# Performance work log

Measured on AMD Instinct MI355X. Metric: run time of the kernel, lower is better.

The kernel has to match this reference:

```python
import jax, jax.numpy as jnp
import numpy as np

LEAKY_ALPHA = 0.2  # LeakyReLU negative slope from init arg `alpha`


def setup_inputs() -> dict:
    key = jax.random.key(0)
    k1, k2, k3, k4 = jax.random.split(key, 4)
    B, N, Fin, Fout = 8, 2048, 256, 256
    h = jax.random.normal(k1, (B, N, Fin), dtype=jnp.float32)
    adj = jax.random.randint(k2, (N, N), 0, 2, dtype=jnp.int32)
    W = jax.random.normal(k3, (Fin, Fout), dtype=jnp.float32) * (1.414 * (6.0 / (Fin + Fout)) ** 0.5)
    a = jax.random.normal(k4, (2 * Fout, 1), dtype=jnp.float32) * (1.414 * (6.0 / (2 * Fout + 1)) ** 0.5)
    return {"h": h, "adj": adj, "W": W, "a": a}


def reference(h, adj, W, a):
    # h: (B, N, Fin), adj: (N, N) int {0,1}, W: (Fin, Fout), a: (2*Fout, 1)
    Fout = W.shape[1]
    Wh = jnp.einsum('bnf,fo->bno', h, W)            # (B, N, Fout)
    a1 = a[:Fout, 0]                                  # attends to target node i
    a2 = a[Fout:, 0]                                  # attends to source node j
    # a^T [Wh_i || Wh_j] == (Wh_i . a1) + (Wh_j . a2); LeakyReLU applied after, as in original
    s_i = Wh @ a1                                     # (B, N)
    s_j = Wh @ a2                                     # (B, N)
    e = jax.nn.leaky_relu(s_i[:, :, None] + s_j[:, None, :], negative_slope=LEAKY_ALPHA)  # (B, N, N)
    N = Wh.shape[1]
    mask = (adj > 0) | jnp.eye(N, dtype=bool)         # adjacency + self-loops
    e = jnp.where(mask[None, :, :], e, -jnp.inf)
    attention = jax.nn.softmax(e, axis=-1)            # dropout is identity in eval
    attention = jnp.nan_to_num(attention, nan=0.0)
    h_prime = jnp.einsum('bij,bjo->bio', attention, Wh)  # (B, N, Fout)
    return jax.nn.elu(h_prime)                        # concat=True -> ELU
```

## Files before the change

kernel.cpp:

```cpp
#include <hip/hip_runtime.h>

typedef unsigned short u16;
typedef unsigned int   u32;
typedef unsigned long long u64;

typedef __bf16 bf16x8 __attribute__((ext_vector_type(8)));
typedef float  f32x4  __attribute__((ext_vector_type(4)));
typedef float  f32x16 __attribute__((ext_vector_type(16)));

#define MFMA_BF16(a,b,c)   __builtin_amdgcn_mfma_f32_16x16x32_bf16((a),(b),(c),0,0,0)
#define MFMA32_BF16(a,b,c) __builtin_amdgcn_mfma_f32_32x32x16_bf16((a),(b),(c),0,0,0)

__device__ __forceinline__ float bf2f(u16 u) {
    return __uint_as_float(((u32)u) << 16);
}
__device__ __forceinline__ u16 f2bf(float x) {
    u32 u = __float_as_uint(x);
    u += 0x7fffu + ((u >> 16) & 1u);
    return (u16)(u >> 16);
}
__device__ __forceinline__ float ldany(const void* p, size_t i, int f32) {
    return f32 ? ((const float*)p)[i] : bf2f(((const u16*)p)[i]);
}
__device__ __forceinline__ int detect_f32(const u32* hw) {
    u32 w = hw[threadIdx.x & 63];
    int e = (w >> 23) & 0xFF;
    u64 m = __ballot(e >= 64 && e <= 190);
    return __popcll(m) >= 32 ? 1 : 0;
}
__device__ __forceinline__ void lbar() {
    asm volatile("s_waitcnt lgkmcnt(0)" ::: "memory");
    __builtin_amdgcn_s_barrier();
}

__global__ __launch_bounds__(256) void kprep0(const void* __restrict__ w, const void* __restrict__ a,
                                              u16* __restrict__ wt, float* __restrict__ wa1,
                                              float* __restrict__ wa2, int* __restrict__ cnt,
                                              const u32* __restrict__ hw) {
    __shared__ float s1[4], s2[4];
    int bid = blockIdx.x, t = threadIdx.x;
    int wid = t >> 6, lane = t & 63;
    if (bid == 0 && t < 8) cnt[t] = 0;
    int f32 = detect_f32(hw);
    int k = bid, o = t;
    float wv = ldany(w, (size_t)k * 256 + o, f32);
    wt[o * 256 + k] = f2bf(wv);
    float p1 = wv * ldany(a, o, f32);
    float p2 = wv * ldany(a, 256 + o, f32);
    for (int d = 32; d; d >>= 1) { p1 += __shfl_down(p1, d); p2 += __shfl_down(p2, d); }
    if (lane == 0) { s1[wid] = p1; s2[wid] = p2; }
    __syncthreads();
    if (o == 0) { wa1[k] = s1[0] + s1[1] + s1[2] + s1[3]; wa2[k] = s2[0] + s2[1] + s2[2] + s2[3]; }
}

struct __align__(16) K2LDS {
    u16 At[64 * 68];
    union { u16 Bt[256 * 68]; u16 Ct[256 * 68]; };
    float wa1s[256], wa2s[256];
    float s1[64], s2[64];
};
__global__ __launch_bounds__(1024, 4) void k2m(const void* __restrict__ h, const u16* __restrict__ wt,
                                               const float* __restrict__ wa1, const float* __restrict__ wa2,
                                               u16* __restrict__ whbt,
                                               float* __restrict__ sig, float* __restrict__ sjg,
                                               const int* __restrict__ adj, u64* __restrict__ mb64) {
    __shared__ K2LDS L;
    int bid = blockIdx.x;
    int t = threadIdx.x;
    int wid = t >> 6, lane = t & 63, ln = lane & 15, qd = lane >> 4;

    if (bid >= 256) {
        int w2 = (bid - 256) * 16 + wid;
        int4 v[8];
        #pragma unroll
        for (int s = 0; s < 8; s++) {
            int task = w2 * 8 + s;
            int row = task >> 3, jb = (task & 7) * 256;
            v[s] = *(const int4*)(adj + (size_t)row * 2048 + jb + lane * 4);
        }
        #pragma unroll
        for (int s = 0; s < 8; s++) {
            int task = w2 * 8 + s;
            int row = task >> 3, jb = (task & 7) * 256;
            int j0 = jb + lane * 4;
            u32 nib = (u32)(v[s].x > 0 || j0     == row)
                    | ((u32)(v[s].y > 0 || j0 + 1 == row) << 1)
                    | ((u32)(v[s].z > 0 || j0 + 2 == row) << 2)
                    | ((u32)(v[s].w > 0 || j0 + 3 == row) << 3);
            u32 sh = 4 * (lane & 7);
            u32 lo = (lane & 8) ? 0u : (nib << sh);
            u32 hi = (lane & 8) ? (nib << sh) : 0u;
            #pragma unroll
            for (int d = 1; d <= 8; d <<= 1) {
                lo |= __shfl_xor(lo, d);
                hi |= __shfl_xor(hi, d);
            }
            if ((lane & 15) == 0)
                mb64[(size_t)row * 32 + (jb >> 6) + (lane >> 4)] =
                    (u64)lo | ((u64)hi << 32);
        }
        return;
    }

    int f32 = detect_f32((const u32*)h);
    int m0 = bid * 64;
    int b  = m0 >> 11;
    int n0 = m0 & 2047;

    if (t < 256) { L.wa1s[t] = wa1[t]; L.wa2s[t] = wa2[t]; }
    if (t < 64) { L.s1[t] = 0.f; L.s2[t] = 0.f; }
    __syncthreads();

    float a1 = 0.f, a2 = 0.f;
    f32x4 acc[4];
    for (int mi = 0; mi < 4; mi++) acc[mi] = (f32x4){0.f, 0.f, 0.f, 0.f};

    for (int c = 0; c < 4; c++) {
        int k0c = c * 64;
        if (t < 512) {
            int r = t >> 3, s = t & 7;
            float xv[8]; u16 uv[8];
            if (f32) {
                const float* src = (const float*)h + (size_t)(m0 + r) * 256 + k0c + s * 8;
                f32x4 x0 = *(const f32x4*)src;
                f32x4 x1 = *(const f32x4*)(src + 4);
                #pragma unroll
                for (int q = 0; q < 4; q++) { xv[q] = x0[q]; xv[4 + q] = x1[q]; }
                #pragma unroll
                for (int q = 0; q < 8; q++) uv[q] = f2bf(xv[q]);
            } else {
                const u16* src = (const u16*)h + (size_t)(m0 + r) * 256 + k0c + s * 8;
                *(uint4*)uv = *(const uint4*)src;
                #pragma unroll
                for (int q = 0; q < 8; q++) xv[q] = bf2f(uv[q]);
            }
            *(uint4*)&L.At[r * 68 + s * 8] = *(uint4*)uv;
            float pa = 0.f, pb = 0.f;
            #pragma unroll
            for (int q = 0; q < 8; q++) {
                pa += xv[q] * L.wa1s[k0c + s * 8 + q];
                pb += xv[q] * L.wa2s[k0c + s * 8 + q];
            }
            a1 += pa; a2 += pb;
        } else {
            int tt = t - 512;
            #pragma unroll
            for (int p = 0; p < 4; p++) {
                int f = (tt >> 3) + p * 64, s = tt & 7;
                *(uint4*)&L.Bt[f * 68 + s * 8] =
                    *(const uint4*)(wt + (size_t)f * 256 + k0c + s * 8);
            }
        }
        __syncthreads();
        for (int ks = 0; ks < 2; ks++) {
            bf16x8 af[4], bfr;
            for (int mi = 0; mi < 4; mi++)
                af[mi] = *(const bf16x8*)&L.At[(mi * 16 + ln) * 68 + ks * 32 + qd * 8];
            bfr = *(const bf16x8*)&L.Bt[(wid * 16 + ln) * 68 + ks * 32 + qd * 8];
            for (int mi = 0; mi < 4; mi++)
                acc[mi] = MFMA_BF16(af[mi], bfr, acc[mi]);
        }
        __syncthreads();
    }

    if (t < 512) {
        atomicAdd(&L.s1[t >> 3], a1);
        atomicAdd(&L.s2[t >> 3], a2);
    }
    for (int mi = 0; mi < 4; mi++) {
        int f = wid * 16 + ln;
        int n = mi * 16 + qd * 4;
        u16 v[4];
        for (int r = 0; r < 4; r++) v[r] = f2bf(acc[mi][r]);
        *(uint2*)&L.Ct[f * 68 + n] = *(uint2*)v;
    }
    __syncthreads();
    if (t < 64) { sig[m0 + t] = L.s1[t]; sjg[m0 + t] = L.s2[t]; }
    {
        int fr = t >> 2, q0 = (t & 3) * 2;
        size_t base = (size_t)b * 524288 + (size_t)fr * 2048 + n0;
        #pragma unroll
        for (int k = 0; k < 2; k++) {
            int s = q0 + k;
            uint4 v = *(uint4*)&L.Ct[fr * 68 + s * 8];
            *(uint4*)(whbt + base + s * 8) = v;
        }
    }
}

struct __align__(16) K4LDS {
    u32   vpack[2048];
    u16   sjb[2048];
    u64   mw[64 * 33];
    float u1[64], u2[64], nsi[64], inv[64];
    float lred[1024];
    u16   Pt[2][8192];
    int   claim[2];
    u32   pad1blk[4096];
};
__global__ __launch_bounds__(1024, 4) void k4(const float* __restrict__ sig,
                                              const float* __restrict__ sjg,
                                              const u64* __restrict__ mb64, const u16* __restrict__ whbt,
                                              void* __restrict__ out, const void* __restrict__ hdet,
                                              int* __restrict__ cnt) {
    __shared__ K4LDS L;
    int f32 = detect_f32((const u32*)hdet);
    int t = threadIdx.x;
    if (t == 0) {
        int xcd = __builtin_amdgcn_s_getreg(63508) & 7;
        int bsel = 0, tile = 0;
        #pragma unroll
        for (int k = 0; k < 8; k++) {
            int bb = (xcd + k) & 7;
            int tt = atomicAdd(&cnt[bb], 1);
            if (tt < 32) { bsel = bb; tile = tt; break; }
        }
        L.claim[0] = bsel; L.claim[1] = tile;
    }
    __syncthreads();
    int b  = L.claim[0];
    int i0 = L.claim[1] * 64;
    int wid = t >> 6, lane = t & 63;
    int l31 = lane & 31, h5 = lane >> 5;
    int fg = wid & 7, ig = wid >> 3;
    const u16* wb = whbt + (size_t)b * 524288 + (size_t)fg * 32 * 2048;
    float lacc = 0.f;

    bf16x8 br[2][8];
    #define LOAD_B(cc, bb) do {                                             \
        int j0_ = (cc) * 128;                                               \
        _Pragma("unroll")                                                   \
        for (int ks = 0; ks < 8; ks++)                                      \
            br[bb][ks] = *(const bf16x8*)(wb +                              \
                (size_t)l31 * 2048 + j0_ + ks * 16 + h5 * 8);               \
    } while (0)

    #define PGEN(cc, bb) do {                                               \
        int r_ = t & 63, o_ = t >> 6;                                       \
        int jb_ = (cc) * 128 + o_ * 8;                                      \
        uint4 pkA_ = *(const uint4*)&L.vpack[jb_];                          \
        uint4 pkB_ = *(const uint4*)&L.vpack[jb_ + 4];                      \
        uint4 sj4_ = *(const uint4*)&L.sjb[jb_];                            \
        u32 mb_ = (u32)(L.mw[r_ * 33 + 2 * (cc) + (o_ >> 3)]                \
                        >> ((o_ & 7) * 8)) & 0xffu;                         \
        float u1_ = L.u1[r_], u2_ = L.u2[r_], nsi_ = L.nsi[r_];             \
        u32 pr_[4];                                                         \
        _Pragma("unroll")                                                   \
        for (int pk = 0; pk < 4; pk++) {                                    \
            u32 vw0_ = (pk == 0) ? pkA_.x : (pk == 1) ? pkA_.z              \
                     : (pk == 2) ? pkB_.x : pkB_.z;                         \
            u32 vw1_ = (pk == 0) ? pkA_.y : (pk == 1) ? pkA_.w              \
                     : (pk == 2) ? pkB_.y : pkB_.w;                         \
            u32 sw_ = (pk == 0) ? sj4_.x : (pk == 1) ? sj4_.y               \
                     : (pk == 2) ? sj4_.z : sj4_.w;                         \
            float sj0_ = __uint_as_float(sw_ << 16);                        \
            float sj1_ = __uint_as_float(sw_ & 0xffff0000u);                \
            float p0_, p1_;                                                 \
            {                                                               \
                bool pos = sj0_ > nsi_;                                     \
                float vv = __uint_as_float(pos ? (vw0_ << 16)               \
                                               : ((vw0_ >> 16) << 16));     \
                p0_ = (pos ? u1_ : u2_) * vv;                               \
                p0_ = ((mb_ >> (2 * pk)) & 1u) ? p0_ : 0.f;                 \
            }                                                               \
            {                                                               \
                bool pos = sj1_ > nsi_;                                     \
                float vv = __uint_as_float(pos ? (vw1_ << 16)               \
                                               : ((vw1_ >> 16) << 16));     \
                p1_ = (pos ? u1_ : u2_) * vv;                               \
                p1_ = ((mb_ >> (2 * pk + 1)) & 1u) ? p1_ : 0.f;             \
            }                                                               \
            lacc += p0_ + p1_;                                              \
            pr_[pk] = __builtin_amdgcn_perm(__float_as_uint(p1_),           \
                                            __float_as_uint(p0_),           \
                                            0x07060302u);                   \
        }                                                                   \
        *(uint4*)&L.Pt[bb][t * 8] = *(uint4*)pr_;                           \
    } while (0)

    LOAD_B(0, 0);
    float sjv0 = sjg[b * 2048 + t];
    float sjv1 = sjg[b * 2048 + 1024 + t];
    {
        float mx = fmaxf(sjv0, sjv1);
        for (int d = 32; d; d >>= 1) mx = fmaxf(mx, __shfl_xor(mx, d));
        if (lane == 0) L.lred[wid] = mx;
    }
    for (int p = 0; p < 2; p++) {
        int idx = t + p * 1024;
        int r = idx >> 5, c = idx & 31;
        L.mw[r * 33 + c] = mb64[(size_t)(i0 + r) * 32 + c];
    }
    __syncthreads();
    float Mb;
    {
        float m0_ = fmaxf(fmaxf(fmaxf(L.lred[0], L.lred[1]), fmaxf(L.lred[2], L.lred[3])),
                          fmaxf(fmaxf(L.lred[4], L.lred[5]), fmaxf(L.lred[6], L.lred[7])));
        float m1_ = fmaxf(fmaxf(fmaxf(L.lred[8], L.lred[9]), fmaxf(L.lred[10], L.lred[11])),
                          fmaxf(fmaxf(L.lred[12], L.lred[13]), fmaxf(L.lred[14], L.lred[15])));
        Mb = fmaxf(m0_, m1_);
    }
    {
        float vj0 = __expf(sjv0 - Mb), v2j0 = __expf(0.2f * (sjv0 - Mb));
        L.vpack[t] = (u32)f2bf(vj0) | ((u32)f2bf(v2j0) << 16);
        L.sjb[t] = f2bf(sjv0);
        float vj1 = __expf(sjv1 - Mb), v2j1 = __expf(0.2f * (sjv1 - Mb));
        L.vpack[t + 1024] = (u32)f2bf(vj1) | ((u32)f2bf(v2j1) << 16);
        L.sjb[t + 1024] = f2bf(sjv1);
    }
    if (t < 64) {
        float siv = sig[b * 2048 + i0 + t];
        float x = siv + Mb;
        float K = fmaxf(x, 0.2f * x);
        L.u1[t] = __expf(x - K);
        L.u2[t] = __expf(0.2f * x - K);
        L.nsi[t] = -siv;
    }
    __syncthreads();
    PGEN(0, 0);

    f32x16 acc;
    #pragma unroll
    for (int q = 0; q < 16; q++) acc[q] = 0.f;

    #define STEP(c, cur, nxt) do {                                          \
        lbar();                                                             \
        if ((c) < 15) { LOAD_B((c) + 1, nxt); PGEN((c) + 1, nxt); }         \
        __builtin_amdgcn_s_setprio(1);                                      \
        _Pragma("unroll")                                                   \
        for (int ks = 0; ks < 8; ks++) {                                    \
            bf16x8 af = *(const bf16x8*)&L.Pt[cur][((ks * 2 + h5) * 64 +    \
                                                    ig * 32 + l31) * 8];    \
            acc = MFMA32_BF16(af, br[cur][ks], acc);                        \
        }                                                                   \
        __builtin_amdgcn_s_setprio(0);                                      \
    } while (0)

    for (int cc = 0; cc < 8; cc++) {
        STEP(2 * cc,     0, 1);
        STEP(2 * cc + 1, 1, 0);
    }

    __syncthreads();
    L.lred[t] = lacc;
    __syncthreads();
    if (t < 64) {
        float s = 0.f;
        #pragma unroll
        for (int q = 0; q < 16; q++) s += L.lred[q * 64 + t];
        L.inv[t] = 1.0f / s;
    }
    __syncthreads();

    {
        int fcol = fg * 32 + l31;
        #pragma unroll
        for (int reg = 0; reg < 16; reg++) {
            int il = ig * 32 + (reg & 3) + 8 * (reg >> 2) + 4 * h5;
            float hp = acc[reg] * L.inv[il];
            float y = hp > 0.f ? hp : (__expf(hp) - 1.f);
            size_t idx = (size_t)(b * 2048 + i0 + il) * 256 + fcol;
            if (f32) ((float*)out)[idx] = y;
            else     ((u16*)out)[idx]   = f2bf(y);
        }
    }
    #undef LOAD_B
    #undef PGEN
    #undef STEP
}

extern "C" void kernel_launch(void* const* d_in, const int* in_sizes, int n_in,
                              void* d_out, int out_size, void* d_ws, size_t ws_size,
                              hipStream_t stream) {
    const void* h   = d_in[0];
    const int*  adj = (const int*)d_in[1];
    const void* W   = d_in[2];
    const void* a   = d_in[3];

    char* ws = (char*)d_ws;
    u16*   WT    = (u16*)  (ws + 0);
    float* si    = (float*)(ws + 131072);
    float* sj    = (float*)(ws + 196608);
    u64*   mb64  = (u64*)  (ws + 557056);
    u16*   whbt  = (u16*)  (ws + 1081344);
    float* Wa1   = (float*)(ws + 9469952);
    float* Wa2   = (float*)(ws + 9470976);
    int*   cnt   = (int*)  (ws + 9472000);

    kprep0<<<dim3(256), dim3(256),  0, stream>>>(W, a, WT, Wa1, Wa2, cnt, (const u32*)h);
    k2m   <<<dim3(384), dim3(1024), 0, stream>>>(h, WT, Wa1, Wa2, whbt, si, sj, adj, mb64);
    k4    <<<dim3(256), dim3(1024), 0, stream>>>(si, sj, mb64, whbt, d_out, h, cnt);
}
```

Before: 161.2 us.

## Move adjacency bitmask packing into prep kernel and simplify k4 barrier

Adjacency-to-bitmask packing moves out of the second kernel into the first prep kernel. It now runs as 2048 small 256-thread blocks doing two tasks per wave, next to the W transpose blocks, so the projection GEMM kernel launches only its 256 tiles. The k4 launch-bounds occupancy hint is dropped, and the custom lgkmcnt-wait-plus-barrier is replaced by __syncthreads. The aim is to stop the mask work from competing with the GEMM tiles and to spread it over more blocks. The risks are a heavier prep kernel and possibly looser register or occupancy settings for k4.

```diff
diff --git a/kernel.cpp b/kernel.cpp
--- a/kernel.cpp
+++ b/kernel.cpp
@@ -28,60 +28,40 @@
     u64 m = __ballot(e >= 64 && e <= 190);
     return __popcll(m) >= 32 ? 1 : 0;
 }
-__device__ __forceinline__ void lbar() {
-    asm volatile("s_waitcnt lgkmcnt(0)" ::: "memory");
-    __builtin_amdgcn_s_barrier();
-}
-
-__global__ __launch_bounds__(256) void kprep0(const void* __restrict__ w, const void* __restrict__ a,
-                                              u16* __restrict__ wt, float* __restrict__ wa1,
-                                              float* __restrict__ wa2, int* __restrict__ cnt,
-                                              const u32* __restrict__ hw) {
+
+__global__ __launch_bounds__(256) void kprep(const void* __restrict__ w, const void* __restrict__ a,
+                                             const int* __restrict__ adj,
+                                             u16* __restrict__ wt, float* __restrict__ wa1,
+                                             float* __restrict__ wa2, u64* __restrict__ mb64,
+                                             int* __restrict__ cnt, const u32* __restrict__ hw) {
     __shared__ float s1[4], s2[4];
     int bid = blockIdx.x, t = threadIdx.x;
     int wid = t >> 6, lane = t & 63;
-    if (bid == 0 && t < 8) cnt[t] = 0;
-    int f32 = detect_f32(hw);
-    int k = bid, o = t;
-    float wv = ldany(w, (size_t)k * 256 + o, f32);
-    wt[o * 256 + k] = f2bf(wv);
-    float p1 = wv * ldany(a, o, f32);
-    float p2 = wv * ldany(a, 256 + o, f32);
-    for (int d = 32; d; d >>= 1) { p1 += __shfl_down(p1, d); p2 += __shfl_down(p2, d); }
-    if (lane == 0) { s1[wid] = p1; s2[wid] = p2; }
-    __syncthreads();
-    if (o == 0) { wa1[k] = s1[0] + s1[1] + s1[2] + s1[3]; wa2[k] = s2[0] + s2[1] + s2[2] + s2[3]; }
-}
-
-struct __align__(16) K2LDS {
-    u16 At[64 * 68];
-    union { u16 Bt[256 * 68]; u16 Ct[256 * 68]; };
-    float wa1s[256], wa2s[256];
-    float s1[64], s2[64];
-};
-__global__ __launch_bounds__(1024, 4) void k2m(const void* __restrict__ h, const u16* __restrict__ wt,
-                                               const float* __restrict__ wa1, const float* __restrict__ wa2,
-                                               u16* __restrict__ whbt,
-                                               float* __restrict__ sig, float* __restrict__ sjg,
-                                               const int* __restrict__ adj, u64* __restrict__ mb64) {
-    __shared__ K2LDS L;
-    int bid = blockIdx.x;
-    int t = threadIdx.x;
-    int wid = t >> 6, lane = t & 63, ln = lane & 15, qd = lane >> 4;
-
-    if (bid >= 256) {
-        int w2 = (bid - 256) * 16 + wid;
-        int4 v[8];
-        #pragma unroll
-        for (int s = 0; s < 8; s++) {
-            int task = w2 * 8 + s;
+    if (bid < 256) {
+        if (bid == 0 && t < 8) cnt[t] = 0;
+        int f32 = detect_f32(hw);
+        int k = bid, o = t;
+        float wv = ldany(w, (size_t)k * 256 + o, f32);
+        wt[o * 256 + k] = f2bf(wv);
+        float p1 = wv * ldany(a, o, f32);
+        float p2 = wv * ldany(a, 256 + o, f32);
+        for (int d = 32; d; d >>= 1) { p1 += __shfl_down(p1, d); p2 += __shfl_down(p2, d); }
+        if (lane == 0) { s1[wid] = p1; s2[wid] = p2; }
+        __syncthreads();
+        if (o == 0) { wa1[k] = s1[0] + s1[1] + s1[2] + s1[3]; wa2[k] = s2[0] + s2[1] + s2[2] + s2[3]; }
+    } else {
+        int w2 = (bid - 256) * 4 + wid;
+        int4 v[2]; int rowv[2], jbv[2];
+        #pragma unroll
+        for (int s = 0; s < 2; s++) {
+            int task = w2 * 2 + s;
             int row = task >> 3, jb = (task & 7) * 256;
+            rowv[s] = row; jbv[s] = jb;
             v[s] = *(const int4*)(adj + (size_t)row * 2048 + jb + lane * 4);
         }
         #pragma unroll
-        for (int s = 0; s < 8; s++) {
-            int task = w2 * 8 + s;
-            int row = task >> 3, jb = (task & 7) * 256;
+        for (int s = 0; s < 2; s++) {
+            int row = rowv[s], jb = jbv[s];
             int j0 = jb + lane * 4;
             u32 nib = (u32)(v[s].x > 0 || j0     == row)
                     | ((u32)(v[s].y > 0 || j0 + 1 == row) << 1)
@@ -99,13 +79,26 @@
                 mb64[(size_t)row * 32 + (jb >> 6) + (lane >> 4)] =
                     (u64)lo | ((u64)hi << 32);
         }
-        return;
-    }
-
+    }
+}
+
+struct __align__(16) K2LDS {
+    u16 At[64 * 68];
+    union { u16 Bt[256 * 68]; u16 Ct[256 * 68]; };
+    float wa1s[256], wa2s[256];
+    float s1[64], s2[64];
+};
+__global__ __launch_bounds__(1024, 4) void k2(const void* __restrict__ h, const u16* __restrict__ wt,
+                                              const float* __restrict__ wa1, const float* __restrict__ wa2,
+                                              u16* __restrict__ whbt,
+                                              float* __restrict__ sig, float* __restrict__ sjg) {
+    __shared__ K2LDS L;
     int f32 = detect_f32((const u32*)h);
-    int m0 = bid * 64;
+    int m0 = blockIdx.x * 64;
     int b  = m0 >> 11;
     int n0 = m0 & 2047;
+    int t = threadIdx.x;
+    int wid = t >> 6, lane = t & 63, ln = lane & 15, qd = lane >> 4;
 
     if (t < 256) { L.wa1s[t] = wa1[t]; L.wa2s[t] = wa2[t]; }
     if (t < 64) { L.s1[t] = 0.f; L.s2[t] = 0.f; }
@@ -198,11 +191,11 @@
     int   claim[2];
     u32   pad1blk[4096];
 };
-__global__ __launch_bounds__(1024, 4) void k4(const float* __restrict__ sig,
-                                              const float* __restrict__ sjg,
-                                              const u64* __restrict__ mb64, const u16* __restrict__ whbt,
-                                              void* __restrict__ out, const void* __restrict__ hdet,
-                                              int* __restrict__ cnt) {
+__global__ __launch_bounds__(1024) void k4(const float* __restrict__ sig,
+                                           const float* __restrict__ sjg,
+                                           const u64* __restrict__ mb64, const u16* __restrict__ whbt,
+                                           void* __restrict__ out, const void* __restrict__ hdet,
+                                           int* __restrict__ cnt) {
     __shared__ K4LDS L;
     int f32 = detect_f32((const u32*)hdet);
     int t = threadIdx.x;
@@ -324,7 +317,7 @@
     for (int q = 0; q < 16; q++) acc[q] = 0.f;
 
     #define STEP(c, cur, nxt) do {                                          \
-        lbar();                                                             \
+        __syncthreads();                                                    \
         if ((c) < 15) { LOAD_B((c) + 1, nxt); PGEN((c) + 1, nxt); }         \
         __builtin_amdgcn_s_setprio(1);                                      \
         _Pragma("unroll")                                                   \
@@ -387,7 +380,7 @@
     float* Wa2   = (float*)(ws + 9470976);
     int*   cnt   = (int*)  (ws + 9472000);
 
-    kprep0<<<dim3(256), dim3(256),  0, stream>>>(W, a, WT, Wa1, Wa2, cnt, (const u32*)h);
-    k2m   <<<dim3(384), dim3(1024), 0, stream>>>(h, WT, Wa1, Wa2, whbt, si, sj, adj, mb64);
-    k4    <<<dim3(256), dim3(1024), 0, stream>>>(si, sj, mb64, whbt, d_out, h, cnt);
-}
+    kprep<<<dim3(2304), dim3(256),  0, stream>>>(W, a, adj, WT, Wa1, Wa2, mb64, cnt, (const u32*)h);
+    k2   <<<dim3(256),  dim3(1024), 0, stream>>>(h, WT, Wa1, Wa2, whbt, si, sj);
+    k4   <<<dim3(256),  dim3(1024), 0, stream>>>(si, sj, mb64, whbt, d_out, h, cnt);
+}
```

Measured after the change: 158.3 us. About the same (-1.8%).
